# Kernel optimization log

Measured on AMD Instinct MI355X. Metric: run time of the kernel, lower is better.

## Reference

```python
import jax, jax.numpy as jnp
import numpy as np

SEQ_LEN = 16384
D = 2048
K = 50          # tagset size
START = 48
STOP = 49
NEG = -10000.0


def setup_inputs() -> dict:
    key = jax.random.key(0)
    k1, k2, k3, k4 = jax.random.split(key, 4)
    input_var = jax.random.normal(k1, (SEQ_LEN, D), jnp.float32)
    tags = jax.random.randint(k2, (SEQ_LEN,), 0, 48, dtype=jnp.int32)  # real tags only
    W = jax.random.normal(k3, (K, D), jnp.float32) * 0.02              # hidden2tag weight
    b = jnp.zeros((K,), jnp.float32)                                   # hidden2tag bias
    transitions = jax.random.normal(k4, (K, K), jnp.float32) * 0.1
    # match the torch init: no transition into START, none out of STOP
    transitions = transitions.at[START, :].set(NEG).at[:, STOP].set(NEG)
    return {"input_var": input_var, "tags": tags, "W": W, "b": b, "transitions": transitions}


def reference(input_var, tags, W, b, transitions):
    # dropout in eval mode == identity (faithful deterministic forward)
    feats = input_var @ W.T + b  # [T, K] emission scores

    # --- CRF forward algorithm (log partition) ---
    alpha0 = jnp.full((K,), NEG, jnp.float32).at[START].set(0.0)

    def step(alpha, feat):
        # tag_var[i, j] = alpha[j] + transitions[i, j] + feat[i]
        s = alpha[None, :] + transitions           # [K, K]
        m = jnp.max(s, axis=1)                     # stable log-sum-exp
        alpha_new = feat + m + jnp.log(jnp.sum(jnp.exp(s - m[:, None]), axis=1))
        return alpha_new, None

    alpha, _ = jax.lax.scan(step, alpha0, feats)
    term = alpha + transitions[STOP]
    mt = jnp.max(term)
    forward_score = mt + jnp.log(jnp.sum(jnp.exp(term - mt)))

    # --- gold path score ---
    pad_start = jnp.concatenate([jnp.array([START], dtype=tags.dtype), tags])
    pad_stop = jnp.concatenate([tags, jnp.array([STOP], dtype=tags.dtype)])
    gold = (jnp.sum(transitions[pad_stop, pad_start])
            + jnp.sum(feats[jnp.arange(SEQ_LEN), tags]))

    return forward_score - gold
```

## Files before the change

kernel.cpp:

```cpp
#include <hip/hip_runtime.h>

typedef unsigned short u16;
typedef unsigned int u32;
typedef __bf16 b16x8 __attribute__((ext_vector_type(8)));
typedef float f32x16 __attribute__((ext_vector_type(16)));

#define SEQ   16384
#define DM    2048
#define KT    50
#define NST   48
#define NSP   49

__device__ __forceinline__ int perm64(int g){
  int q = (g>>2)&3;
  return (q==1 || q==2) ? (g^12) : g;
}
__device__ __forceinline__ u16 bfb(float f){
  __bf16 b = (__bf16)f;
  return __builtin_bit_cast(u16, b);
}
__device__ __forceinline__ int pk2(float a, float b){
  return (int)((u32)bfb(a) | ((u32)bfb(b) << 16));
}
__device__ __forceinline__ b16x8 cast8(int4 v){ return __builtin_bit_cast(b16x8, v); }

__device__ __forceinline__ f32x16 mfma_(b16x8 a, b16x8 b, f32x16 c){
  return __builtin_amdgcn_mfma_f32_32x32x16_bf16(a, b, c, 0, 0, 0);
}

__device__ __forceinline__ void mm64(const b16x8 A[2][4], const b16x8 B[4][2], f32x16 acc[2][2]){
#pragma unroll
  for (int mi=0; mi<2; ++mi)
#pragma unroll
    for (int ni=0; ni<2; ++ni){
      f32x16 a;
#pragma unroll
      for (int q=0;q<16;q++) a[q] = 0.0f;
#pragma unroll
      for (int kt=0; kt<4; ++kt) a = mfma_(A[mi][kt], B[kt][ni], a);
      acc[mi][ni] = a;
    }
}

__device__ __forceinline__ void repack(const f32x16 acc[2][2], b16x8 B[4][2]){
#pragma unroll
  for (int kb=0; kb<4; ++kb){
    const int mi = kb>>1, t = kb&1;
#pragma unroll
    for (int ni=0; ni<2; ++ni){
      int4 dw;
      dw.x = pk2(acc[mi][ni][8*t+0], acc[mi][ni][8*t+1]);
      dw.y = pk2(acc[mi][ni][8*t+2], acc[mi][ni][8*t+3]);
      dw.z = pk2(acc[mi][ni][8*t+4], acc[mi][ni][8*t+5]);
      dw.w = pk2(acc[mi][ni][8*t+6], acc[mi][ni][8*t+7]);
      B[kb][ni] = cast8(dw);
    }
  }
}
__device__ __forceinline__ void repack_s(const f32x16 acc[2][2], b16x8 B[4][2], float s){
#pragma unroll
  for (int kb=0; kb<4; ++kb){
    const int mi = kb>>1, t = kb&1;
#pragma unroll
    for (int ni=0; ni<2; ++ni){
      int4 dw;
      dw.x = pk2(acc[mi][ni][8*t+0]*s, acc[mi][ni][8*t+1]*s);
      dw.y = pk2(acc[mi][ni][8*t+2]*s, acc[mi][ni][8*t+3]*s);
      dw.z = pk2(acc[mi][ni][8*t+4]*s, acc[mi][ni][8*t+5]*s);
      dw.w = pk2(acc[mi][ni][8*t+6]*s, acc[mi][ni][8*t+7]*s);
      B[kb][ni] = cast8(dw);
    }
  }
}

template<int PERM>
__device__ __forceinline__ void ident_frags(b16x8 B[4][2], int lane){
  const int h = lane>>5, j0 = lane&31;
#pragma unroll
  for (int kt=0; kt<4; ++kt)
#pragma unroll
    for (int ni=0; ni<2; ++ni){
      const int col = j0 + 32*ni;
      int d[4];
#pragma unroll
      for (int dd=0; dd<4; ++dd){
        int r0 = 16*kt + 8*h + 2*dd, r1 = r0 + 1;
        int p0 = PERM ? perm64(r0) : r0;
        int p1 = PERM ? perm64(r1) : r1;
        d[dd] = (int)((p0==col ? 0x3F80u : 0u) | ((p1==col ? 0x3F80u : 0u) << 16));
      }
      int4 v; v.x=d[0]; v.y=d[1]; v.z=d[2]; v.w=d[3];
      B[kt][ni] = cast8(v);
    }
}

__device__ __forceinline__ float acc_wave_max(const f32x16 acc[2][2]){
  float m = 0.0f;
#pragma unroll
  for (int mi=0;mi<2;mi++)
#pragma unroll
    for (int ni=0;ni<2;ni++)
#pragma unroll
      for (int q=0;q<16;q++) m = fmaxf(m, acc[mi][ni][q]);
#pragma unroll
  for (int o=32;o>=1;o>>=1) m = fmaxf(m, __shfl_xor(m, o, 64));
  return m;
}

template<int PROW>
__device__ __forceinline__ void store_mat_lds(u16* mat, const f32x16 acc[2][2], float inv, int lane){
  const int h = lane>>5, j0 = lane&31;
#pragma unroll
  for (int mi=0;mi<2;mi++)
#pragma unroll
    for (int ni=0;ni<2;ni++)
#pragma unroll
      for (int r=0;r<16;r++){
        int gp = 32*mi + (r&3) + 8*(r>>2) + 4*h;
        int a = PROW ? perm64(gp) : gp;
        int b = perm64(32*ni + j0);
        mat[a*64 + (b ^ ((a&7)<<3))] = bfb(acc[mi][ni][r]*inv);
      }
}
template<int PROW>
__device__ __forceinline__ void store_mat_glob(u16* mat, const f32x16 acc[2][2], float inv, int lane){
  const int h = lane>>5, j0 = lane&31;
#pragma unroll
  for (int mi=0;mi<2;mi++)
#pragma unroll
    for (int ni=0;ni<2;ni++)
#pragma unroll
      for (int r=0;r<16;r++){
        int gp = 32*mi + (r&3) + 8*(r>>2) + 4*h;
        int a = PROW ? perm64(gp) : gp;
        int b = perm64(32*ni + j0);
        mat[a*64 + b] = bfb(acc[mi][ni][r]*inv);
      }
}
__device__ __forceinline__ void load_afrag_lds(const u16* mat, b16x8 A[2][4], int lane){
  const int h = lane>>5, i0 = lane&31;
#pragma unroll
  for (int mi=0;mi<2;mi++)
#pragma unroll
    for (int kt=0;kt<4;kt++){
      int i = 32*mi + i0;
      int cb = (16*kt + 8*h) ^ ((i&7)<<3);
      A[mi][kt] = cast8(*(const int4*)(mat + i*64 + cb));
    }
}
__device__ __forceinline__ void load_afrag_glob(const u16* mat, b16x8 A[2][4], int lane){
  const int h = lane>>5, i0 = lane&31;
#pragma unroll
  for (int mi=0;mi<2;mi++)
#pragma unroll
    for (int kt=0;kt<4;kt++){
      int i = 32*mi + i0;
      A[mi][kt] = cast8(*(const int4*)(mat + i*64 + 16*kt + 8*h));
    }
}

__global__ __launch_bounds__(512, 2) void k_gemm(const float* __restrict__ in,
      const int* __restrict__ tags, const float* __restrict__ W,
      const float* __restrict__ bias, const float* __restrict__ T,
      float* __restrict__ feats, float* __restrict__ gpart, int* __restrict__ counter){
  __shared__ __align__(16) char smem[65536];
  u16* const bA = (u16*)smem;
  u16* const bB = (u16*)(smem + 32768);
  const int t = threadIdx.x;
  const int w = t>>6, lane = t&63;
  const int j0 = lane&31, h = lane>>5;
  const int rh = w&1, ch = (w>>1)&1, kq = (w>>2)&1;
  const int row0 = blockIdx.x*64;
  const int aswz = (j0&7)<<3;
  if (blockIdx.x==0 && t==0) *counter = 0;

  float rA[2][8], rB[2][8];
  f32x16 acc;
#pragma unroll
  for (int q=0;q<16;q++) acc[q]=0.f;

#define LOADCHUNK(kc)                                                       \
  { _Pragma("unroll")                                                       \
    for (int i=0;i<2;i++){                                                  \
      int g=(i<<9)+t; int r=g>>4, c8=g&15;                                  \
      const float* p = in + (size_t)(row0+r)*DM + (kc)*128 + c8*8;          \
      float4 f0=*(const float4*)p, f1=*(const float4*)(p+4);                \
      rA[i][0]=f0.x; rA[i][1]=f0.y; rA[i][2]=f0.z; rA[i][3]=f0.w;           \
      rA[i][4]=f1.x; rA[i][5]=f1.y; rA[i][6]=f1.z; rA[i][7]=f1.w;           \
      if (r < KT){                                                          \
        const float* q2 = W + (size_t)r*DM + (kc)*128 + c8*8;               \
        float4 g0=*(const float4*)q2, g1=*(const float4*)(q2+4);            \
        rB[i][0]=g0.x; rB[i][1]=g0.y; rB[i][2]=g0.z; rB[i][3]=g0.w;         \
        rB[i][4]=g1.x; rB[i][5]=g1.y; rB[i][6]=g1.z; rB[i][7]=g1.w;         \
      } else {                                                              \
        _Pragma("unroll") for (int z=0;z<8;z++) rB[i][z]=0.f;               \
      }                                                                     \
    } }
#define WRITECHUNK(d)                                                       \
  { _Pragma("unroll")                                                       \
    for (int i=0;i<2;i++){                                                  \
      int g=(i<<9)+t; int r=g>>4, c8=g&15;                                  \
      int off = r*128 + ((c8*8) ^ ((r&7)<<3));                              \
      int4 da; da.x=pk2(rA[i][0],rA[i][1]); da.y=pk2(rA[i][2],rA[i][3]);    \
      da.z=pk2(rA[i][4],rA[i][5]); da.w=pk2(rA[i][6],rA[i][7]);             \
      *(int4*)(bA + (d)*8192 + off) = da;                                   \
      int4 db; db.x=pk2(rB[i][0],rB[i][1]); db.y=pk2(rB[i][2],rB[i][3]);    \
      db.z=pk2(rB[i][4],rB[i][5]); db.w=pk2(rB[i][6],rB[i][7]);             \
      *(int4*)(bB + (d)*8192 + off) = db;                                   \
    } }

  LOADCHUNK(0); WRITECHUNK(0);
  __syncthreads();
  for (int kc=0; kc<16; ++kc){
    const int d = kc & 1;
    if (kc < 15) LOADCHUNK(kc+1);
    const u16* Arow = bA + d*8192 + (32*rh + j0)*128;
    const u16* Brow = bB + d*8192 + (32*ch + j0)*128;
#pragma unroll
    for (int kk=0;kk<4;kk++){
      const int kt = kq*4 + kk;
      b16x8 aF = cast8(*(const int4*)(Arow + ((kt*16 + h*8) ^ aswz)));
      b16x8 bF = cast8(*(const int4*)(Brow + ((kt*16 + h*8) ^ aswz)));
      acc = mfma_(aF, bF, acc);
    }
    if (kc < 15) WRITECHUNK(d^1);
    __syncthreads();
  }
#undef LOADCHUNK
#undef WRITECHUNK

  float* planes = (float*)smem;
  float* tile   = (float*)(smem + 32768);
  float* mrow   = (float*)(smem + 49664);
#pragma unroll
  for (int r=0;r<16;r++){
    int gp = (r&3) + 8*(r>>2) + 4*h;
    planes[kq*4096 + (32*rh + gp)*64 + 32*ch + j0] = acc[r];
  }
  __syncthreads();
  for (int cidx = t; cidx < 4096; cidx += 512){
    int g = cidx>>6, c = cidx&63;
    float v = planes[cidx] + planes[4096 + cidx];
    tile[g*66+c] = (c<KT) ? (v + bias[c]) : -1e4f;
  }
  __syncthreads();
  if (t < 64){
    int g = t;
    float mx = -1e30f;
    for (int c=0;c<KT;c++) mx = fmaxf(mx, tile[g*66+c]);
    mrow[g] = mx;
    int tt = row0 + g;
    int s1 = tags[tt];
    int s0 = (tt==0) ? NST : tags[tt-1];
    float part = (tile[g*66 + s1] - mx) + T[s1*50 + s0];
    if (tt == SEQ-1) part += T[NSP*50 + s1];
#pragma unroll
    for (int o=32;o>=1;o>>=1) part += __shfl_xor(part, o, 64);
    if (t==0) gpart[blockIdx.x] = part;
  }
  __syncthreads();
  for (int cidx = t; cidx < 4096; cidx += 512){
    int g = cidx>>6, c = cidx&63;
    feats[(size_t)(row0+g)*64 + c] = (c<KT) ? (tile[g*66+c] - mrow[g]) : -1e4f;
  }
}

__global__ __launch_bounds__(512, 2) void k_scan(const float* __restrict__ feats,
        const float* __restrict__ T, const float* __restrict__ gpart,
        int* __restrict__ counter, u16* __restrict__ M1, float* __restrict__ S1,
        float* __restrict__ out){
  const int t = threadIdx.x;
  const int w = t>>6, lane = t&63;
  const int h = lane>>5;
  const int blk = blockIdx.x;
  __shared__ __align__(16) u16 E_lds[4096];
  __shared__ __align__(16) u16 mats[8][4096];
  __shared__ float logs[8];
  __shared__ float alpha[64];
  __shared__ int bcast;

  for (int idx = t; idx < 4096; idx += 512){
    int a = idx>>6, b = idx&63;
    int pa = perm64(a);
    float v = (pa<KT && b<KT) ? __expf(T[pa*50 + b]) : 0.f;
    E_lds[a*64 + (b ^ ((a&7)<<3))] = bfb(v);
  }
  __syncthreads();

  b16x8 Ef[2][4];
  load_afrag_lds(E_lds, Ef, lane);
  float E32[2][4][8];
#pragma unroll
  for (int mi=0;mi<2;mi++)
#pragma unroll
    for (int kt=0;kt<4;kt++)
#pragma unroll
      for (int j=0;j<8;j++) E32[mi][kt][j] = (float)Ef[mi][kt][j];

  b16x8 Bf[4][2];
  ident_frags<0>(Bf, lane);
  const int p0 = perm64(lane & 31);
  const int t0 = (blk*8 + w)*16;
  float x0a = feats[(size_t)t0*64 + p0];
  float x1a = feats[(size_t)t0*64 + 32 + p0];
  float x0b = feats[(size_t)(t0+1)*64 + p0];
  float x1b = feats[(size_t)(t0+1)*64 + 32 + p0];
  f32x16 acc[2][2];
#pragma unroll 1
  for (int s=0;s<16;s++){
    float u0 = __expf(x0a), u1 = __expf(x1a);
    x0a = x0b; x1a = x1b;
    if (s<14){
      x0b = feats[(size_t)(t0+s+2)*64 + p0];
      x1b = feats[(size_t)(t0+s+2)*64 + 32 + p0];
    }
    b16x8 Af[2][4];
#pragma unroll
    for (int mi=0;mi<2;mi++){
      const float uu = mi ? u1 : u0;
#pragma unroll
      for (int kt=0;kt<4;kt++){
        int4 dw;
        dw.x = pk2(uu*E32[mi][kt][0], uu*E32[mi][kt][1]);
        dw.y = pk2(uu*E32[mi][kt][2], uu*E32[mi][kt][3]);
        dw.z = pk2(uu*E32[mi][kt][4], uu*E32[mi][kt][5]);
        dw.w = pk2(uu*E32[mi][kt][6], uu*E32[mi][kt][7]);
        Af[mi][kt] = cast8(dw);
      }
    }
    mm64(Af, Bf, acc);
    repack(acc, Bf);
  }
  float m = acc_wave_max(acc);
  store_mat_lds<1>(mats[w], acc, 1.0f/m, lane);
  if (lane==0) logs[w] = __logf(m);
  __syncthreads();
  if (w==0){
    float slog = logs[0]+logs[1]+logs[2]+logs[3]+logs[4]+logs[5]+logs[6]+logs[7];
    b16x8 Bc[4][2]; ident_frags<1>(Bc, lane);
    f32x16 a2[2][2];
#pragma unroll 1
    for (int m8=0;m8<8;m8++){
      b16x8 Am[2][4];
      load_afrag_lds(mats[m8], Am, lane);
      mm64(Am, Bc, a2);
      repack(a2, Bc);
    }
    float m2 = acc_wave_max(a2);
    slog += __logf(m2);
    store_mat_glob<0>(M1 + (size_t)blk*4096, a2, 1.0f/m2, lane);
    if (lane==0) S1[blk] = slog;
  }
  __syncthreads();
  if (t==0){
    __threadfence();
    bcast = atomicAdd(counter, 1);
  }
  __syncthreads();
  if (bcast != gridDim.x - 1) return;
  __threadfence();

  {
    b16x8 Bc[4][2]; ident_frags<1>(Bc, lane);
    f32x16 a2[2][2];
    float sl = 0.f;
    b16x8 A0[2][4], A1[2][4], A2[2][4];
    load_afrag_glob(M1 + (size_t)(w*16+0)*4096, A0, lane);
    load_afrag_glob(M1 + (size_t)(w*16+1)*4096, A1, lane);
#pragma unroll 1
    for (int mm=0; mm<16; mm++){
      if (mm<14) load_afrag_glob(M1 + (size_t)(w*16+mm+2)*4096, A2, lane);
      sl += S1[w*16+mm];
      mm64(A0, Bc, a2);
      if (mm==7){
        float mx = acc_wave_max(a2);
        sl += __logf(mx);
        repack_s(a2, Bc, 1.0f/mx);
      } else {
        repack(a2, Bc);
      }
#pragma unroll
      for (int mi=0;mi<2;mi++)
#pragma unroll
        for (int kt=0;kt<4;kt++){ A0[mi][kt] = A1[mi][kt]; A1[mi][kt] = A2[mi][kt]; }
    }
    float mx = acc_wave_max(a2);
    sl += __logf(mx);
    store_mat_lds<0>(mats[w], a2, 1.0f/mx, lane);
    if (lane==0) logs[w] = sl;
  }
  __syncthreads();
  if (w==0){
    b16x8 Bc[4][2]; ident_frags<1>(Bc, lane);
    f32x16 a2[2][2];
#pragma unroll 1
    for (int m8=0;m8<8;m8++){
      b16x8 Am[2][4];
      load_afrag_lds(mats[m8], Am, lane);
      mm64(Am, Bc, a2);
      repack(a2, Bc);
    }
    float slog = logs[0]+logs[1]+logs[2]+logs[3]+logs[4]+logs[5]+logs[6]+logs[7];
    if ((lane&31)==16){
#pragma unroll
      for (int mi=0;mi<2;mi++)
#pragma unroll
        for (int r=0;r<16;r++){
          int gp = 32*mi + (r&3) + 8*(r>>2) + 4*h;
          alpha[gp] = a2[mi][1][r];
        }
    }
    float gold = gpart[lane] + gpart[lane+64] + gpart[lane+128] + gpart[lane+192];
#pragma unroll
    for (int o=32;o>=1;o>>=1) gold += __shfl_xor(gold, o, 64);
    float a = alpha[lane];
    float term = (lane < KT && a > 0.f) ? (__logf(a) + slog + T[NSP*50 + lane]) : -1e30f;
    float tm = term;
#pragma unroll
    for (int o=32;o>=1;o>>=1) tm = fmaxf(tm, __shfl_xor(tm, o, 64));
    float e = __expf(term - tm);
#pragma unroll
    for (int o=32;o>=1;o>>=1) e += __shfl_xor(e, o, 64);
    if (lane==0) out[0] = (tm + __logf(e)) - gold;
  }
}

extern "C" void kernel_launch(void* const* d_in, const int* in_sizes, int n_in,
                              void* d_out, int out_size, void* d_ws, size_t ws_size,
                              hipStream_t stream) {
  (void)in_sizes; (void)n_in; (void)out_size; (void)ws_size;
  const float* input = (const float*)d_in[0];
  const int*   tags  = (const int*)  d_in[1];
  const float* W     = (const float*)d_in[2];
  const float* bias  = (const float*)d_in[3];
  const float* T     = (const float*)d_in[4];

  char* ws = (char*)d_ws;
  float* feats   = (float*)(ws + 0);
  float* gpart   = (float*)(ws + 4194304);
  int*   counter = (int*)  (ws + 4195328);
  u16*   M1      = (u16*)  (ws + 4195840);
  float* S1      = (float*)(ws + 5244416);

  k_gemm<<<256, 512, 0, stream>>>(input, tags, W, bias, T, feats, gpart, counter);
  k_scan<<<128, 512, 0, stream>>>(feats, T, gpart, counter, M1, S1, (float*)d_out);
}
```

Measured before the change: 104.7 us.

## Fuse emission GEMM with per-block CRF scan and split final reduction kernel

Folds the per-chunk CRF transfer-matrix products into the GEMM kernel, reading emissions from shared memory instead of writing a feats buffer to global memory and reading it back. Each 64-row block now produces its own 64x64 chunk matrix. A separate single-block kernel then chains the 256 chunk matrices, replacing the atomic-counter last-block pattern. LDS use grows to 128KB per block, which may reduce occupancy, and the final serial chain doubles to 32 matrices per wave.

```diff
diff --git a/kernel.cpp b/kernel.cpp
--- a/kernel.cpp
+++ b/kernel.cpp
@@ -159,20 +159,20 @@
     }
 }
 
-__global__ __launch_bounds__(512, 2) void k_gemm(const float* __restrict__ in,
+__global__ __launch_bounds__(512, 2) void k_fused(const float* __restrict__ in,
       const int* __restrict__ tags, const float* __restrict__ W,
       const float* __restrict__ bias, const float* __restrict__ T,
-      float* __restrict__ feats, float* __restrict__ gpart, int* __restrict__ counter){
-  __shared__ __align__(16) char smem[65536];
+      float* __restrict__ gpart, u16* __restrict__ M1, float* __restrict__ S1){
+  __shared__ __align__(16) char smem[131072];
   u16* const bA = (u16*)smem;
   u16* const bB = (u16*)(smem + 32768);
+  __shared__ float logs[8];
   const int t = threadIdx.x;
   const int w = t>>6, lane = t&63;
   const int j0 = lane&31, h = lane>>5;
   const int rh = w&1, ch = (w>>1)&1, kq = (w>>2)&1;
   const int row0 = blockIdx.x*64;
   const int aswz = (j0&7)<<3;
-  if (blockIdx.x==0 && t==0) *counter = 0;
 
   float rA[2][8], rB[2][8];
   f32x16 acc;
@@ -232,16 +232,32 @@
   float* planes = (float*)smem;
   float* tile   = (float*)(smem + 32768);
   float* mrow   = (float*)(smem + 49664);
+  u16*   mats   = (u16*)  (smem + 65536);
 #pragma unroll
   for (int r=0;r<16;r++){
     int gp = (r&3) + 8*(r>>2) + 4*h;
     planes[kq*4096 + (32*rh + gp)*64 + 32*ch + j0] = acc[r];
   }
+  float E32[2][4][8];
+  {
+    const int pr = perm64(j0);
+#pragma unroll
+    for (int mi=0;mi<2;mi++){
+      const int prow = 32*mi + pr;
+#pragma unroll
+      for (int kt=0;kt<4;kt++)
+#pragma unroll
+        for (int j=0;j<8;j++){
+          const int c = 16*kt + 8*h + j;
+          E32[mi][kt][j] = (prow < KT && c < KT) ? __expf(T[prow*50 + c]) : 0.f;
+        }
+    }
+  }
   __syncthreads();
   for (int cidx = t; cidx < 4096; cidx += 512){
     int g = cidx>>6, c = cidx&63;
     float v = planes[cidx] + planes[4096 + cidx];
-    tile[g*66+c] = (c<KT) ? (v + bias[c]) : -1e4f;
+    tile[g*66 + c] = (c<KT) ? (v + bias[c]) : -1e4f;
   }
   __syncthreads();
   if (t < 64){
@@ -259,81 +275,43 @@
     if (t==0) gpart[blockIdx.x] = part;
   }
   __syncthreads();
-  for (int cidx = t; cidx < 4096; cidx += 512){
-    int g = cidx>>6, c = cidx&63;
-    feats[(size_t)(row0+g)*64 + c] = (c<KT) ? (tile[g*66+c] - mrow[g]) : -1e4f;
-  }
-}
-
-__global__ __launch_bounds__(512, 2) void k_scan(const float* __restrict__ feats,
-        const float* __restrict__ T, const float* __restrict__ gpart,
-        int* __restrict__ counter, u16* __restrict__ M1, float* __restrict__ S1,
-        float* __restrict__ out){
-  const int t = threadIdx.x;
-  const int w = t>>6, lane = t&63;
-  const int h = lane>>5;
-  const int blk = blockIdx.x;
-  __shared__ __align__(16) u16 E_lds[4096];
-  __shared__ __align__(16) u16 mats[8][4096];
-  __shared__ float logs[8];
-  __shared__ float alpha[64];
-  __shared__ int bcast;
-
-  for (int idx = t; idx < 4096; idx += 512){
-    int a = idx>>6, b = idx&63;
-    int pa = perm64(a);
-    float v = (pa<KT && b<KT) ? __expf(T[pa*50 + b]) : 0.f;
-    E_lds[a*64 + (b ^ ((a&7)<<3))] = bfb(v);
-  }
-  __syncthreads();
-
-  b16x8 Ef[2][4];
-  load_afrag_lds(E_lds, Ef, lane);
-  float E32[2][4][8];
-#pragma unroll
-  for (int mi=0;mi<2;mi++)
-#pragma unroll
-    for (int kt=0;kt<4;kt++)
-#pragma unroll
-      for (int j=0;j<8;j++) E32[mi][kt][j] = (float)Ef[mi][kt][j];
-
-  b16x8 Bf[4][2];
-  ident_frags<0>(Bf, lane);
-  const int p0 = perm64(lane & 31);
-  const int t0 = (blk*8 + w)*16;
-  float x0a = feats[(size_t)t0*64 + p0];
-  float x1a = feats[(size_t)t0*64 + 32 + p0];
-  float x0b = feats[(size_t)(t0+1)*64 + p0];
-  float x1b = feats[(size_t)(t0+1)*64 + 32 + p0];
-  f32x16 acc[2][2];
+
+  {
+    b16x8 Bf[4][2];
+    ident_frags<0>(Bf, lane);
+    const int pr = perm64(j0);
+    const int tr0 = w*8;
+    float x0 = tile[tr0*66 + pr]      - mrow[tr0];
+    float x1 = tile[tr0*66 + 32 + pr] - mrow[tr0];
+    f32x16 sacc[2][2];
 #pragma unroll 1
-  for (int s=0;s<16;s++){
-    float u0 = __expf(x0a), u1 = __expf(x1a);
-    x0a = x0b; x1a = x1b;
-    if (s<14){
-      x0b = feats[(size_t)(t0+s+2)*64 + p0];
-      x1b = feats[(size_t)(t0+s+2)*64 + 32 + p0];
-    }
-    b16x8 Af[2][4];
-#pragma unroll
-    for (int mi=0;mi<2;mi++){
-      const float uu = mi ? u1 : u0;
-#pragma unroll
-      for (int kt=0;kt<4;kt++){
-        int4 dw;
-        dw.x = pk2(uu*E32[mi][kt][0], uu*E32[mi][kt][1]);
-        dw.y = pk2(uu*E32[mi][kt][2], uu*E32[mi][kt][3]);
-        dw.z = pk2(uu*E32[mi][kt][4], uu*E32[mi][kt][5]);
-        dw.w = pk2(uu*E32[mi][kt][6], uu*E32[mi][kt][7]);
-        Af[mi][kt] = cast8(dw);
-      }
-    }
-    mm64(Af, Bf, acc);
-    repack(acc, Bf);
-  }
-  float m = acc_wave_max(acc);
-  store_mat_lds<1>(mats[w], acc, 1.0f/m, lane);
-  if (lane==0) logs[w] = __logf(m);
+    for (int s=0;s<8;s++){
+      float u0 = __expf(x0), u1 = __expf(x1);
+      if (s<7){
+        x0 = tile[(tr0+s+1)*66 + pr]      - mrow[tr0+s+1];
+        x1 = tile[(tr0+s+1)*66 + 32 + pr] - mrow[tr0+s+1];
+      }
+      b16x8 Af[2][4];
+#pragma unroll
+      for (int mi=0;mi<2;mi++){
+        const float uu = mi ? u1 : u0;
+#pragma unroll
+        for (int kt=0;kt<4;kt++){
+          int4 dw;
+          dw.x = pk2(uu*E32[mi][kt][0], uu*E32[mi][kt][1]);
+          dw.y = pk2(uu*E32[mi][kt][2], uu*E32[mi][kt][3]);
+          dw.z = pk2(uu*E32[mi][kt][4], uu*E32[mi][kt][5]);
+          dw.w = pk2(uu*E32[mi][kt][6], uu*E32[mi][kt][7]);
+          Af[mi][kt] = cast8(dw);
+        }
+      }
+      mm64(Af, Bf, sacc);
+      repack(sacc, Bf);
+    }
+    float m = acc_wave_max(sacc);
+    store_mat_lds<1>(mats + w*4096, sacc, 1.0f/m, lane);
+    if (lane==0) logs[w] = __logf(m);
+  }
   __syncthreads();
   if (w==0){
     float slog = logs[0]+logs[1]+logs[2]+logs[3]+logs[4]+logs[5]+logs[6]+logs[7];
@@ -342,37 +320,42 @@
 #pragma unroll 1
     for (int m8=0;m8<8;m8++){
       b16x8 Am[2][4];
-      load_afrag_lds(mats[m8], Am, lane);
+      load_afrag_lds(mats + m8*4096, Am, lane);
       mm64(Am, Bc, a2);
       repack(a2, Bc);
     }
     float m2 = acc_wave_max(a2);
     slog += __logf(m2);
-    store_mat_glob<0>(M1 + (size_t)blk*4096, a2, 1.0f/m2, lane);
-    if (lane==0) S1[blk] = slog;
-  }
-  __syncthreads();
-  if (t==0){
-    __threadfence();
-    bcast = atomicAdd(counter, 1);
-  }
-  __syncthreads();
-  if (bcast != gridDim.x - 1) return;
-  __threadfence();
+    store_mat_glob<0>(M1 + (size_t)blockIdx.x*4096, a2, 1.0f/m2, lane);
+    if (lane==0) S1[blockIdx.x] = slog;
+  }
+}
+
+__global__ __launch_bounds__(512, 2) void k_final(const u16* __restrict__ M1,
+      const float* __restrict__ S1, const float* __restrict__ T,
+      const float* __restrict__ gpart, float* __restrict__ out){
+  const int t = threadIdx.x;
+  const int w = t>>6, lane = t&63;
+  const int h = lane>>5;
+  __shared__ __align__(16) u16 mats[8][4096];
+  __shared__ float logs[8];
+  __shared__ float alpha[64];
 
   {
+    const int base = w*32;
     b16x8 Bc[4][2]; ident_frags<1>(Bc, lane);
     f32x16 a2[2][2];
     float sl = 0.f;
-    b16x8 A0[2][4], A1[2][4], A2[2][4];
-    load_afrag_glob(M1 + (size_t)(w*16+0)*4096, A0, lane);
-    load_afrag_glob(M1 + (size_t)(w*16+1)*4096, A1, lane);
+    b16x8 A0[2][4], A1[2][4], A2[2][4], A3[2][4];
+    load_afrag_glob(M1 + (size_t)(base+0)*4096, A0, lane);
+    load_afrag_glob(M1 + (size_t)(base+1)*4096, A1, lane);
+    load_afrag_glob(M1 + (size_t)(base+2)*4096, A2, lane);
 #pragma unroll 1
-    for (int mm=0; mm<16; mm++){
-      if (mm<14) load_afrag_glob(M1 + (size_t)(w*16+mm+2)*4096, A2, lane);
-      sl += S1[w*16+mm];
+    for (int mm=0; mm<32; mm++){
+      if (mm<29) load_afrag_glob(M1 + (size_t)(base+mm+3)*4096, A3, lane);
+      sl += S1[base+mm];
       mm64(A0, Bc, a2);
-      if (mm==7){
+      if (mm!=31 && (mm&7)==7){
         float mx = acc_wave_max(a2);
         sl += __logf(mx);
         repack_s(a2, Bc, 1.0f/mx);
@@ -382,7 +365,9 @@
 #pragma unroll
       for (int mi=0;mi<2;mi++)
 #pragma unroll
-        for (int kt=0;kt<4;kt++){ A0[mi][kt] = A1[mi][kt]; A1[mi][kt] = A2[mi][kt]; }
+        for (int kt=0;kt<4;kt++){
+          A0[mi][kt]=A1[mi][kt]; A1[mi][kt]=A2[mi][kt]; A2[mi][kt]=A3[mi][kt];
+        }
     }
     float mx = acc_wave_max(a2);
     sl += __logf(mx);
@@ -436,12 +421,10 @@
   const float* T     = (const float*)d_in[4];
 
   char* ws = (char*)d_ws;
-  float* feats   = (float*)(ws + 0);
-  float* gpart   = (float*)(ws + 4194304);
-  int*   counter = (int*)  (ws + 4195328);
-  u16*   M1      = (u16*)  (ws + 4195840);
-  float* S1      = (float*)(ws + 5244416);
-
-  k_gemm<<<256, 512, 0, stream>>>(input, tags, W, bias, T, feats, gpart, counter);
-  k_scan<<<128, 512, 0, stream>>>(feats, T, gpart, counter, M1, S1, (float*)d_out);
-}
+  float* gpart = (float*)(ws + 0);
+  u16*   M1    = (u16*)  (ws + 1024);
+  float* S1    = (float*)(ws + 2098176);
+
+  k_fused<<<256, 512, 0, stream>>>(input, tags, W, bias, T, gpart, M1, S1);
+  k_final<<<1,   512, 0, stream>>>(M1, S1, T, gpart, (float*)d_out);
+}
```

After: 121.6 us. 16.1% more time.
